# Kernel tuning notes

Hardware: AMD Instinct MI355X
Metric: run time of the kernel (lower is better)

Reference implementation:

```python
import jax, jax.numpy as jnp
from jax import lax
import numpy as np

B, T, IN, H, NC = 2048, 512, 1, 128, 8


def setup_inputs() -> dict:
    key = jax.random.key(0)
    ks = jax.random.split(key, 13)
    s = 0.05
    inp = {
        "x": jax.random.normal(ks[0], (B, T, IN), dtype=jnp.float32),
        # layer 0 LSTM params (PyTorch layout: W_ih [4H, in], W_hh [4H, H])
        "W_ih0": jax.random.normal(ks[1], (4 * H, IN), dtype=jnp.float32) * s,
        "W_hh0": jax.random.normal(ks[2], (4 * H, H), dtype=jnp.float32) * s,
        "b_ih0": jax.random.normal(ks[3], (4 * H,), dtype=jnp.float32) * s,
        "b_hh0": jax.random.normal(ks[4], (4 * H,), dtype=jnp.float32) * s,
        # layer 1 LSTM params
        "W_ih1": jax.random.normal(ks[5], (4 * H, H), dtype=jnp.float32) * s,
        "W_hh1": jax.random.normal(ks[6], (4 * H, H), dtype=jnp.float32) * s,
        "b_ih1": jax.random.normal(ks[7], (4 * H,), dtype=jnp.float32) * s,
        "b_hh1": jax.random.normal(ks[8], (4 * H,), dtype=jnp.float32) * s,
        # classifier: Linear(H,64) -> ReLU -> Linear(64,NC)
        "W1": jax.random.normal(ks[9], (64, H), dtype=jnp.float32) * s,
        "b1": jax.random.normal(ks[10], (64,), dtype=jnp.float32) * s,
        "W2": jax.random.normal(ks[11], (NC, 64), dtype=jnp.float32) * s,
        "b2": jax.random.normal(ks[12], (NC,), dtype=jnp.float32) * s,
    }
    return inp


def _lstm_layer(x_seq, W_ih, W_hh, b_ih, b_hh):
    # x_seq: [B, T, in]. PyTorch gate order: i, f, g, o.
    bsz = x_seq.shape[0]
    h_dim = W_hh.shape[1]
    # Precompute input projections for all timesteps (big GEMM outside scan).
    x_proj = jnp.einsum('bti,gi->btg', x_seq, W_ih) + b_ih + b_hh  # [B, T, 4H]

    def step(carry, xp_t):
        h, c = carry
        gates = xp_t + h @ W_hh.T  # [B, 4H]
        i_g, f_g, g_g, o_g = jnp.split(gates, 4, axis=-1)
        i_g = jax.nn.sigmoid(i_g)
        f_g = jax.nn.sigmoid(f_g)
        g_g = jnp.tanh(g_g)
        o_g = jax.nn.sigmoid(o_g)
        c = f_g * c + i_g * g_g
        h = o_g * jnp.tanh(c)
        return (h, c), h

    init = (jnp.zeros((bsz, h_dim), x_seq.dtype), jnp.zeros((bsz, h_dim), x_seq.dtype))
    (_, _), hs = lax.scan(step, init, jnp.swapaxes(x_proj, 0, 1))  # hs: [T, B, H]
    return jnp.swapaxes(hs, 0, 1)  # [B, T, H]


def reference(x, W_ih0, W_hh0, b_ih0, b_hh0, W_ih1, W_hh1, b_ih1, b_hh1, W1, b1, W2, b2):
    h0 = _lstm_layer(x, W_ih0, W_hh0, b_ih0, b_hh0)   # [B, T, H]
    h1 = _lstm_layer(h0, W_ih1, W_hh1, b_ih1, b_hh1)  # [B, T, H] (dropout off in eval)
    last = h1[:, -1, :]                                # [B, H]
    hidden = jax.nn.relu(last @ W1.T + b1)             # [B, 64]
    logits = hidden @ W2.T + b2                        # [B, NC]
    return logits
```

## Files before the change

### kernel.cpp

```cpp
#include <hip/hip_runtime.h>
#include <stdint.h>

typedef float f32x4 __attribute__((ext_vector_type(4)));
typedef short s16x8 __attribute__((ext_vector_type(8)));
typedef short s16x4 __attribute__((ext_vector_type(4)));
typedef uint32_t u32x4 __attribute__((ext_vector_type(4)));

#define HDIM 128
#define TLEN 512
#define BT 16

__device__ __forceinline__ unsigned short f2bf(float f) {
    union { float f; uint32_t u; } v; v.f = f;
    uint32_t r = v.u + 0x7FFFu + ((v.u >> 16) & 1u);
    return (unsigned short)(r >> 16);
}
__device__ __forceinline__ float bfhi(uint32_t u){ union{uint32_t u;float f;}v; v.u = u & 0xFFFF0000u; return v.f; }
__device__ __forceinline__ float bflo(uint32_t u){ union{uint32_t u;float f;}v; v.u = u << 16; return v.f; }
__device__ __forceinline__ float bf2f(short s){ union{uint32_t u;float f;}v; v.u = ((uint32_t)(unsigned short)s) << 16; return v.f; }

__device__ __forceinline__ float sigmoidf_(float x){
    float e = __expf(-x);
    return __builtin_amdgcn_rcpf(1.0f + e);
}
__device__ __forceinline__ float tanhf_(float x){
    float e = __expf(2.0f * x);
    return 1.0f - 2.0f * __builtin_amdgcn_rcpf(1.0f + e);
}

#define MFMA16(A, B, C) __builtin_amdgcn_mfma_f32_16x16x32_bf16((A), (B), (C), 0, 0, 0)
#define UNPK(arr, idx) (((idx) & 1) ? bfhi(arr[(idx) >> 1]) : bflo(arr[(idx) >> 1]))

__global__ __launch_bounds__(512, 2) void lstm_pipe_kernel(
    const float* __restrict__ x,
    const float* __restrict__ Wih0,
    const float* __restrict__ Whh0,
    const float* __restrict__ bih0,
    const float* __restrict__ bhh0,
    const float* __restrict__ Wih1,
    const float* __restrict__ Whh1,
    const float* __restrict__ bih1,
    const float* __restrict__ bhh1,
    const float* __restrict__ W1,
    const float* __restrict__ b1,
    const float* __restrict__ W2,
    const float* __restrict__ b2,
    short* __restrict__ ring,
    int* __restrict__ flags,
    float* __restrict__ out)
{
    __shared__ __align__(16) short h0A[2][2048];
    __shared__ __align__(16) short h1f[2][2048];
    __shared__ __align__(16) float headH[16 * HDIM];
    __shared__ __align__(16) float headL[16 * 64];

    const int role = blockIdx.x & 1;
    const int p    = blockIdx.x >> 1;
    const int tid  = threadIdx.x;
    const int w = tid >> 6;
    const int l = tid & 63;
    const int n = l & 15;
    const int q = l >> 4;
    const int b0 = p * BT;
    const float* xrow = x + (size_t)(b0 + n) * TLEN;
    short* ringp = ring + (size_t)p * TLEN * 2048;

    const int u0 = w * 16 + q * 4;
    const int fragoff = (((u0 >> 5) * 64) + n + 16 * ((u0 >> 3) & 3)) * 8 + (u0 & 7);

    if (role == 0) {
        s16x8 w0f[4][4];
        #pragma unroll
        for (int c = 0; c < 4; ++c) {
            #pragma unroll
            for (int tile = 0; tile < 4; ++tile) {
                const int g  = tile * 128 + w * 16 + n;
                const int k0 = c * 32 + q * 8;
                const float* pw = Whh0 + g * HDIM + k0;
                s16x8 a;
                #pragma unroll
                for (int j = 0; j < 8; ++j) a[j] = (short)f2bf(pw[j]);
                w0f[c][tile] = a;
            }
        }
        uint32_t b0p[8], wxp[8];
        #pragma unroll
        for (int i = 0; i < 8; ++i) {
            const int tr0 = 2 * i;
            const int tile = tr0 >> 2, r0 = tr0 & 3;
            const int g0 = tile * 128 + u0 + r0;
            const int g1 = g0 + 1;
            b0p[i] = ((uint32_t)f2bf(bih0[g1] + bhh0[g1]) << 16) | f2bf(bih0[g0] + bhh0[g0]);
            wxp[i] = ((uint32_t)f2bf(Wih0[g1]) << 16) | f2bf(Wih0[g0]);
        }
        float c0v[4] = {0.f, 0.f, 0.f, 0.f};

        {
            const float x0 = xrow[0];
            s16x4 hw;
            #pragma unroll
            for (int r = 0; r < 4; ++r) {
                const float pi = fmaf(UNPK(wxp, r),      x0, UNPK(b0p, r));
                const float pg = fmaf(UNPK(wxp, 8 + r),  x0, UNPK(b0p, 8 + r));
                const float po = fmaf(UNPK(wxp, 12 + r), x0, UNPK(b0p, 12 + r));
                const float ig = sigmoidf_(pi);
                const float gg = tanhf_(pg);
                const float og = sigmoidf_(po);
                const float cc = ig * gg;
                c0v[r] = cc;
                hw[r] = (short)f2bf(og * tanhf_(cc));
            }
            *(s16x4*)&h0A[0][fragoff] = hw;
            *(s16x4*)&ringp[fragoff] = hw;
        }
        __syncthreads();

        #pragma unroll 1
        for (int i = 0; i < 511; ++i) {
            const short* R = h0A[i & 1];
            short*       W = h0A[(i + 1) & 1];
            const float xv = xrow[i + 1];
            s16x8 hb[4];
            #pragma unroll
            for (int c = 0; c < 4; ++c) hb[c] = *(const s16x8*)&R[(c * 64 + l) * 8];
            f32x4 a[4];
            #pragma unroll
            for (int tile = 0; tile < 4; ++tile) {
                #pragma unroll
                for (int r = 0; r < 4; ++r) {
                    const int tr = tile * 4 + r;
                    a[tile][r] = fmaf(UNPK(wxp, tr), xv, UNPK(b0p, tr));
                }
            }
            #pragma unroll
            for (int c = 0; c < 4; ++c) {
                #pragma unroll
                for (int tile = 0; tile < 4; ++tile)
                    a[tile] = MFMA16(w0f[c][tile], hb[c], a[tile]);
            }
            s16x4 hw;
            #pragma unroll
            for (int r = 0; r < 4; ++r) {
                const float ig = sigmoidf_(a[0][r]);
                const float fg = sigmoidf_(a[1][r]);
                const float gg = tanhf_(a[2][r]);
                const float og = sigmoidf_(a[3][r]);
                const float cc = fmaf(fg, c0v[r], ig * gg);
                c0v[r] = cc;
                hw[r] = (short)f2bf(og * tanhf_(cc));
            }
            *(s16x4*)&W[fragoff] = hw;
            *(s16x4*)&ringp[(size_t)(i + 1) * 2048 + fragoff] = hw;

            if (((i + 2) & 7) == 0) {
                __threadfence();
                __syncthreads();
                if (tid == 0)
                    __hip_atomic_store(&flags[p], (i + 2) >> 3,
                                       __ATOMIC_RELEASE, __HIP_MEMORY_SCOPE_AGENT);
            } else {
                __syncthreads();
            }
        }
        return;
    }

    s16x8 wi1f[4][4], wh1f[4][4];
    #pragma unroll
    for (int c = 0; c < 4; ++c) {
        #pragma unroll
        for (int tile = 0; tile < 4; ++tile) {
            const int g  = tile * 128 + w * 16 + n;
            const int k0 = c * 32 + q * 8;
            const float* p1 = Wih1 + g * HDIM + k0;
            const float* p2 = Whh1 + g * HDIM + k0;
            s16x8 a, b;
            #pragma unroll
            for (int j = 0; j < 8; ++j) { a[j] = (short)f2bf(p1[j]); b[j] = (short)f2bf(p2[j]); }
            wi1f[c][tile] = a; wh1f[c][tile] = b;
        }
    }
    uint32_t b1p[8];
    #pragma unroll
    for (int i = 0; i < 8; ++i) {
        const int tr0 = 2 * i;
        const int tile = tr0 >> 2, r0 = tr0 & 3;
        const int g0 = tile * 128 + u0 + r0;
        const int g1 = g0 + 1;
        b1p[i] = ((uint32_t)f2bf(bih1[g1] + bhh1[g1]) << 16) | f2bf(bih1[g0] + bhh1[g0]);
    }
    for (int s2 = tid; s2 < 1024; s2 += 512) ((uint32_t*)h1f[1])[s2] = 0u;
    float c1v[4] = {0.f, 0.f, 0.f, 0.f};

#define WAITCHUNK(C) do {                                                     \
    if (tid == 0) {                                                           \
        while (__hip_atomic_load(&flags[p], __ATOMIC_ACQUIRE,                 \
                                 __HIP_MEMORY_SCOPE_AGENT) < (C))             \
            __builtin_amdgcn_s_sleep(8);                                      \
    }                                                                         \
    __syncthreads();                                                          \
    __threadfence();         \
} while (0)

#define LOADCUR(DST, T) do {                                                  \
    _Pragma("unroll")                                                         \
    for (int c = 0; c < 4; ++c)                                               \
        (DST)[c] = *(const s16x8*)&ringp[(size_t)(T) * 2048 + (c * 64 + l) * 8]; \
} while (0)

#define BSTEP(K, CUR, NXT, DO_PF) do {                                        \
    const short* R1_ = h1f[((K) + 1) & 1];                                    \
    short*       W1_ = h1f[(K) & 1];                                          \
    s16x8 hb1_[4];                                                            \
    _Pragma("unroll")                                                         \
    for (int c = 0; c < 4; ++c) hb1_[c] = *(const s16x8*)&R1_[(c * 64 + l) * 8]; \
    f32x4 a_[4];                                                              \
    _Pragma("unroll")                                                         \
    for (int tile = 0; tile < 4; ++tile) {                                    \
        _Pragma("unroll")                                                     \
        for (int r = 0; r < 4; ++r) a_[tile][r] = UNPK(b1p, tile * 4 + r);    \
    }                                                                         \
    _Pragma("unroll")                                                         \
    for (int c = 0; c < 4; ++c) {                                             \
        _Pragma("unroll")                                                     \
        for (int tile = 0; tile < 4; ++tile)                                  \
            a_[tile] = MFMA16(wi1f[c][tile], (CUR)[c], a_[tile]);             \
    }                                                                         \
    if (DO_PF) { LOADCUR(NXT, (K) + 1); }                                     \
    _Pragma("unroll")                                                         \
    for (int c = 0; c < 4; ++c) {                                             \
        _Pragma("unroll")                                                     \
        for (int tile = 0; tile < 4; ++tile)                                  \
            a_[tile] = MFMA16(wh1f[c][tile], hb1_[c], a_[tile]);              \
    }                                                                         \
    s16x4 hw_;                                                                \
    _Pragma("unroll")                                                         \
    for (int r = 0; r < 4; ++r) {                                             \
        const float ig = sigmoidf_(a_[0][r]);                                 \
        const float fg = sigmoidf_(a_[1][r]);                                 \
        const float gg = tanhf_(a_[2][r]);                                    \
        const float og = sigmoidf_(a_[3][r]);                                 \
        const float cc = fmaf(fg, c1v[r], ig * gg);                           \
        c1v[r] = cc;                                                          \
        hw_[r] = (short)f2bf(og * tanhf_(cc));                                \
    }                                                                         \
    *(s16x4*)&W1_[fragoff] = hw_;                                             \
    __syncthreads();                                                          \
} while (0)

    s16x8 curA[4], curB[4];

    #pragma unroll 1
    for (int c64 = 0; c64 < 63; ++c64) {
        WAITCHUNK(c64 + 1);
        const int kb = 8 * c64;
        LOADCUR(curA, kb);
        BSTEP(kb + 0, curA, curB, true);
        BSTEP(kb + 1, curB, curA, true);
        BSTEP(kb + 2, curA, curB, true);
        BSTEP(kb + 3, curB, curA, true);
        BSTEP(kb + 4, curA, curB, true);
        BSTEP(kb + 5, curB, curA, true);
        BSTEP(kb + 6, curA, curB, true);
        BSTEP(kb + 7, curB, curA, false);
    }
    WAITCHUNK(64);
    LOADCUR(curA, 504);
    BSTEP(504, curA, curB, true);
    BSTEP(505, curB, curA, true);
    BSTEP(506, curA, curB, true);
    BSTEP(507, curB, curA, true);
    BSTEP(508, curA, curB, true);
    BSTEP(509, curB, curA, true);
    BSTEP(510, curA, curB, true);

    {
        const short* R1 = h1f[0];
        s16x8 hb1_[4];
        #pragma unroll
        for (int c = 0; c < 4; ++c) hb1_[c] = *(const s16x8*)&R1[(c * 64 + l) * 8];
        f32x4 a_[4];
        #pragma unroll
        for (int tile = 0; tile < 4; ++tile) {
            #pragma unroll
            for (int r = 0; r < 4; ++r) a_[tile][r] = UNPK(b1p, tile * 4 + r);
        }
        #pragma unroll
        for (int c = 0; c < 4; ++c) {
            #pragma unroll
            for (int tile = 0; tile < 4; ++tile) {
                a_[tile] = MFMA16(wi1f[c][tile], curB[c], a_[tile]);
                a_[tile] = MFMA16(wh1f[c][tile], hb1_[c], a_[tile]);
            }
        }
        f32x4 hv;
        #pragma unroll
        for (int r = 0; r < 4; ++r) {
            const float ig = sigmoidf_(a_[0][r]);
            const float fg = sigmoidf_(a_[1][r]);
            const float gg = tanhf_(a_[2][r]);
            const float og = sigmoidf_(a_[3][r]);
            const float cc = fmaf(fg, c1v[r], ig * gg);
            hv[r] = og * tanhf_(cc);
        }
        *(f32x4*)&headH[n * HDIM + u0] = hv;
    }
    __syncthreads();

    #pragma unroll
    for (int rep = 0; rep < 2; ++rep) {
        const int idx = tid + rep * 512;
        const int nn = idx >> 6, j = idx & 63;
        float s = b1[j];
        const float* wrow = W1 + j * HDIM;
        const float* hrow = headH + nn * HDIM;
        #pragma unroll
        for (int k = 0; k < HDIM; k += 4) {
            const f32x4 hv = *(const f32x4*)&hrow[k];
            const f32x4 wv = *(const f32x4*)&wrow[k];
            s += hv[0]*wv[0] + hv[1]*wv[1] + hv[2]*wv[2] + hv[3]*wv[3];
        }
        headL[nn * 64 + j] = fmaxf(s, 0.0f);
    }
    __syncthreads();

    if (tid < 128) {
        const int nn = tid >> 3, cls = tid & 7;
        float s = b2[cls];
        const float* wrow = W2 + cls * 64;
        const float* hrow = headL + nn * 64;
        #pragma unroll
        for (int k = 0; k < 64; k += 4) {
            const f32x4 hv = *(const f32x4*)&hrow[k];
            const f32x4 wv = *(const f32x4*)&wrow[k];
            s += hv[0]*wv[0] + hv[1]*wv[1] + hv[2]*wv[2] + hv[3]*wv[3];
        }
        out[(size_t)(b0 + nn) * 8 + cls] = s;
    }
#undef WAITCHUNK
#undef LOADCUR
#undef BSTEP
}

__global__ __launch_bounds__(512, 2) void lstm_fused_kernel(
    const float* __restrict__ x,
    const float* __restrict__ Wih0,
    const float* __restrict__ Whh0,
    const float* __restrict__ bih0,
    const float* __restrict__ bhh0,
    const float* __restrict__ Wih1,
    const float* __restrict__ Whh1,
    const float* __restrict__ bih1,
    const float* __restrict__ bhh1,
    const float* __restrict__ W1,
    const float* __restrict__ b1,
    const float* __restrict__ W2,
    const float* __restrict__ b2,
    float* __restrict__ out)
{
    __shared__ __align__(16) short wh1lds[65536];
    __shared__ __align__(16) short h0f0[2048], h0f1[2048];
    __shared__ __align__(16) short h1f0[2048], h1f1[2048];
    __shared__ __align__(16) float b1lds[4][8][16];

    const int tid = threadIdx.x;
    const int w   = tid >> 6;
    const int wl  = w & 3;
    const bool isL0 = (w < 4);
    const int l = tid & 63;
    const int n = l & 15;
    const int q = l >> 4;
    const int b0 = blockIdx.x * BT;
    const float* xrow = x + (size_t)(b0 + n) * TLEN;

    for (int s2 = tid; s2 < 8192; s2 += 512) {
        const int ll = s2 & 63, t2 = (s2 >> 6) & 7, cc = (s2 >> 9) & 3, wv = s2 >> 11;
        const int row = (t2 >> 1) * 128 + 32 * wv + 16 * (t2 & 1) + (ll & 15);
        const int k0  = cc * 32 + (ll >> 4) * 8;
        const float* p = Whh1 + row * HDIM + k0;
        s16x8 a;
        #pragma unroll
        for (int j = 0; j < 8; ++j) a[j] = (short)f2bf(p[j]);
        *(s16x8*)&wh1lds[s2 * 8] = a;
    }
    {
        const int idx = tid;
        const int wv = idx >> 7, t2 = (idx >> 4) & 7, j = idx & 15;
        const int row = (t2 >> 1) * 128 + 32 * wv + 16 * (t2 & 1) + j;
        b1lds[wv][t2][j] = bih1[row] + bhh1[row];
    }
    for (int s2 = tid; s2 < 1024; s2 += 512) ((uint32_t*)h1f1)[s2] = 0u;

    const int ub0 = 32 * wl + 4 * q;
    const int ub1 = ub0 + 16;
    const int fo0 = ((ub0 >> 5) * 64 + n + 16 * ((ub0 >> 3) & 3)) * 8 + (ub0 & 7);
    const int fo1 = ((ub1 >> 5) * 64 + n + 16 * ((ub1 >> 3) & 3)) * 8 + (ub1 & 7);

#define L0ITER(K, R0, W0) do {                                                \
    const int xi_ = (K) + 1;                                                  \
    const float xv_ = xrow[xi_ < TLEN ? xi_ : (TLEN - 1)];                    \
    s16x8 hb_[4];                                                             \
    _Pragma("unroll")                                                         \
    for (int c = 0; c < 4; ++c) hb_[c] = *(const s16x8*)&(R0)[(c * 64 + l) * 8]; \
    f32x4 a_[8];                                                              \
    _Pragma("unroll")                                                         \
    for (int t2 = 0; t2 < 8; ++t2) {                                          \
        _Pragma("unroll")                                                     \
        for (int r = 0; r < 4; ++r)                                           \
            a_[t2][r] = fmaf(bfhi(bwx[t2][r]), xv_, bflo(bwx[t2][r]));        \
    }                                                                         \
    _Pragma("unroll")                                                         \
    for (int c = 0; c < 4; ++c) {                                             \
        _Pragma("unroll")                                                     \
        for (int t2 = 0; t2 < 8; ++t2)                                        \
            a_[t2] = MFMA16(w0f[c][t2], hb_[c], a_[t2]);                      \
    }                                                                         \
    _Pragma("unroll")                                                         \
    for (int h = 0; h < 2; ++h) {                                             \
        s16x4 hw;                                                             \
        _Pragma("unroll")                                                     \
        for (int r = 0; r < 4; ++r) {                                         \
            const float ig = sigmoidf_(a_[0 + h][r]);                         \
            const float fg = sigmoidf_(a_[2 + h][r]);                         \
            const float gg = tanhf_(a_[4 + h][r]);                            \
            const float og = sigmoidf_(a_[6 + h][r]);                         \
            const float cc = fmaf(fg, c0_[h][r], ig * gg);                    \
            c0_[h][r] = cc;                                                   \
            hw[r] = (short)f2bf(og * tanhf_(cc));                             \
        }                                                                     \
        *(s16x4*)&(W0)[h ? fo1 : fo0] = hw;                                   \
    }                                                                         \
    __syncthreads();                                                          \
} while (0)

#define L1ITER(K, R0, R1, W1) do {                                            \
    s16x8 hb0_[4], hb1_[4];                                                   \
    _Pragma("unroll")                                                         \
    for (int c = 0; c < 4; ++c) {                                             \
        hb0_[c] = *(const s16x8*)&(R0)[(c * 64 + l) * 8];                     \
        hb1_[c] = *(const s16x8*)&(R1)[(c * 64 + l) * 8];                     \
    }                                                                         \
    f32x4 a_[8];                                                              \
    _Pragma("unroll")                                                         \
    for (int t2 = 0; t2 < 8; ++t2)                                            \
        a_[t2] = *(const f32x4*)&b1lds[wl][t2][q * 4];                        \
    _Pragma("unroll")                                                         \
    for (int c = 0; c < 4; ++c) {                                             \
        _Pragma("unroll")                                                     \
        for (int t2 = 0; t2 < 8; ++t2)                                        \
            a_[t2] = MFMA16(wi1f[c][t2], hb0_[c], a_[t2]);                    \
    }                                                                         \
    _Pragma("unroll")                                                         \
    for (int c = 0; c < 4; ++c) {                                             \
        s16x8 wt_[8];                                                         \
        _Pragma("unroll")                                                     \
        for (int t2 = 0; t2 < 8; ++t2)                                        \
            wt_[t2] = *(const s16x8*)&wh1lds[(((wl * 4 + c) * 8 + t2) * 64 + l) * 8]; \
        _Pragma("unroll")                                                     \
        for (int t2 = 0; t2 < 8; ++t2)                                        \
            a_[t2] = MFMA16(wt_[t2], hb1_[c], a_[t2]);                        \
    }                                                                         \
    _Pragma("unroll")                                                         \
    for (int h = 0; h < 2; ++h) {                                             \
        s16x4 hw;                                                             \
        _Pragma("unroll")                                                     \
        for (int r = 0; r < 4; ++r) {                                         \
            const float ig = sigmoidf_(a_[0 + h][r]);                         \
            const float fg = sigmoidf_(a_[2 + h][r]);                         \
            const float gg = tanhf_(a_[4 + h][r]);                            \
            const float og = sigmoidf_(a_[6 + h][r]);                         \
            const float cc = fmaf(fg, c1_[h][r], ig * gg);                    \
            c1_[h][r] = cc;                                                   \
            hw[r] = (short)f2bf(og * tanhf_(cc));                             \
        }                                                                     \
        *(s16x4*)&(W1)[h ? fo1 : fo0] = hw;                                   \
    }                                                                         \
    __syncthreads();                                                          \
} while (0)

    if (isL0) {
        s16x8 w0f[4][8];
        #pragma unroll
        for (int c = 0; c < 4; ++c) {
            #pragma unroll
            for (int t2 = 0; t2 < 8; ++t2) {
                const int row = (t2 >> 1) * 128 + 32 * wl + 16 * (t2 & 1) + n;
                const int k0 = c * 32 + q * 8;
                const float* p = Whh0 + row * HDIM + k0;
                s16x8 a;
                #pragma unroll
                for (int j = 0; j < 8; ++j) a[j] = (short)f2bf(p[j]);
                w0f[c][t2] = a;
            }
        }
        u32x4 bwx[8];
        #pragma unroll
        for (int t2 = 0; t2 < 8; ++t2) {
            #pragma unroll
            for (int r = 0; r < 4; ++r) {
                const int row = (t2 >> 1) * 128 + 32 * wl + 16 * (t2 & 1) + 4 * q + r;
                bwx[t2][r] = ((uint32_t)f2bf(Wih0[row]) << 16) | f2bf(bih0[row] + bhh0[row]);
            }
        }
        float c0_[2][4] = {{0.f,0.f,0.f,0.f},{0.f,0.f,0.f,0.f}};
        {
            const float x0 = xrow[0];
            #pragma unroll
            for (int h = 0; h < 2; ++h) {
                s16x4 hw;
                #pragma unroll
                for (int r = 0; r < 4; ++r) {
                    const float pi = fmaf(bfhi(bwx[0 + h][r]), x0, bflo(bwx[0 + h][r]));
                    const float pg = fmaf(bfhi(bwx[4 + h][r]), x0, bflo(bwx[4 + h][r]));
                    const float po = fmaf(bfhi(bwx[6 + h][r]), x0, bflo(bwx[6 + h][r]));
                    const float ig = sigmoidf_(pi);
                    const float gg = tanhf_(pg);
                    const float og = sigmoidf_(po);
                    const float cc = ig * gg;
                    c0_[h][r] = cc;
                    hw[r] = (short)f2bf(og * tanhf_(cc));
                }
                *(s16x4*)&h0f0[h ? fo1 : fo0] = hw;
            }
        }
        __syncthreads();
        #pragma unroll 1
        for (int k = 0; k < TLEN; k += 2) {
            L0ITER(k,     h0f0, h0f1);
            L0ITER(k + 1, h0f1, h0f0);
        }
    } else {
        s16x8 wi1f[4][8];
        #pragma unroll
        for (int c = 0; c < 4; ++c) {
            #pragma unroll
            for (int t2 = 0; t2 < 8; ++t2) {
                const int row = (t2 >> 1) * 128 + 32 * wl + 16 * (t2 & 1) + n;
                const int k0 = c * 32 + q * 8;
                const float* p = Wih1 + row * HDIM + k0;
                s16x8 a;
                #pragma unroll
                for (int j = 0; j < 8; ++j) a[j] = (short)f2bf(p[j]);
                wi1f[c][t2] = a;
            }
        }
        float c1_[2][4] = {{0.f,0.f,0.f,0.f},{0.f,0.f,0.f,0.f}};
        __syncthreads();
        #pragma unroll 1
        for (int k = 0; k < TLEN; k += 2) {
            L1ITER(k,     h0f0, h1f1, h1f0);
            L1ITER(k + 1, h0f1, h1f0, h1f1);
        }
        {
            const short* R0 = h0f0;
            const short* R1 = h1f1;
            (void)R0; (void)R1;
        }
    }

    __syncthreads();

    float* headH = (float*)wh1lds;
    float* headL = headH + 16 * HDIM;
    if (!isL0) {
        #pragma unroll
        for (int h = 0; h < 2; ++h) {
            const s16x4 hv = *(const s16x4*)&h1f1[h ? fo1 : fo0];
            f32x4 hf;
            #pragma unroll
            for (int r = 0; r < 4; ++r) hf[r] = bf2f(hv[r]);
            *(f32x4*)&headH[n * HDIM + (h ? ub1 : ub0)] = hf;
        }
    }
    __syncthreads();

    #pragma unroll
    for (int rep = 0; rep < 2; ++rep) {
        const int idx = tid + rep * 512;
        const int nn = idx >> 6, j = idx & 63;
        float s = b1[j];
        const float* wrow = W1 + j * HDIM;
        const float* hrow = headH + nn * HDIM;
        #pragma unroll
        for (int k = 0; k < HDIM; k += 4) {
            const f32x4 hv = *(const f32x4*)&hrow[k];
            const f32x4 wv = *(const f32x4*)&wrow[k];
            s += hv[0]*wv[0] + hv[1]*wv[1] + hv[2]*wv[2] + hv[3]*wv[3];
        }
        headL[nn * 64 + j] = fmaxf(s, 0.0f);
    }
    __syncthreads();

    if (tid < 128) {
        const int nn = tid >> 3, cls = tid & 7;
        float s = b2[cls];
        const float* wrow = W2 + cls * 64;
        const float* hrow = headL + nn * 64;
        #pragma unroll
        for (int k = 0; k < 64; k += 4) {
            const f32x4 hv = *(const f32x4*)&hrow[k];
            const f32x4 wv = *(const f32x4*)&wrow[k];
            s += hv[0]*wv[0] + hv[1]*wv[1] + hv[2]*wv[2] + hv[3]*wv[3];
        }
        out[(size_t)(b0 + nn) * 8 + cls] = s;
    }
#undef L0ITER
#undef L1ITER
}

extern "C" void kernel_launch(void* const* d_in, const int* in_sizes, int n_in,
                              void* d_out, int out_size, void* d_ws, size_t ws_size,
                              hipStream_t stream) {
    const float* x    = (const float*)d_in[0];
    const float* Wih0 = (const float*)d_in[1];
    const float* Whh0 = (const float*)d_in[2];
    const float* bih0 = (const float*)d_in[3];
    const float* bhh0 = (const float*)d_in[4];
    const float* Wih1 = (const float*)d_in[5];
    const float* Whh1 = (const float*)d_in[6];
    const float* bih1 = (const float*)d_in[7];
    const float* bhh1 = (const float*)d_in[8];
    const float* W1   = (const float*)d_in[9];
    const float* b1   = (const float*)d_in[10];
    const float* W2   = (const float*)d_in[11];
    const float* b2   = (const float*)d_in[12];
    float* outp = (float*)d_out;

    const size_t ring_bytes = (size_t)128 * TLEN * 2048 * sizeof(short);
    const size_t need = 4096 + ring_bytes;

    if (ws_size >= need) {
        int*   flags = (int*)d_ws;
        short* ring  = (short*)((char*)d_ws + 4096);
        hipMemsetAsync(d_ws, 0, 4096, stream);
        lstm_pipe_kernel<<<256, 512, 0, stream>>>(
            x, Wih0, Whh0, bih0, bhh0, Wih1, Whh1, bih1, bhh1,
            W1, b1, W2, b2, ring, flags, outp);
    } else {
        lstm_fused_kernel<<<128, 512, 0, stream>>>(
            x, Wih0, Whh0, bih0, bhh0, Wih1, Whh1, bih1, bhh1,
            W1, b1, W2, b2, outp);
    }
}
```

Before: 954.8 us.

## Replace full-length layer-0 ring with bounded circular buffer plus consumer back-pressure

The layer-0 to layer-1 handoff buffer is now a power-of-two circular ring of D chunks sized from the available workspace, instead of storing all 512 timesteps per batch tile. A consumer flag lets the layer-1 block post progress, and the layer-0 producer waits on it before overwriting slots. Flags are padded to separate 64-byte lines and the spin-wait sleep is shortened. The aim is a smaller, more cache-resident ring and less flag contention, at the cost of possible producer stalls and bounded spin loops that could break out early if the limit is reached.

```diff
diff --git a/kernel.cpp b/kernel.cpp
--- a/kernel.cpp
+++ b/kernel.cpp
@@ -9,6 +9,7 @@
 #define HDIM 128
 #define TLEN 512
 #define BT 16
+#define SPIN_LIMIT (1 << 22)
 
 __device__ __forceinline__ unsigned short f2bf(float f) {
     union { float f; uint32_t u; } v; v.f = f;
@@ -46,8 +47,11 @@
     const float* __restrict__ W2,
     const float* __restrict__ b2,
     short* __restrict__ ring,
-    int* __restrict__ flags,
-    float* __restrict__ out)
+    int* __restrict__ prodF,
+    int* __restrict__ consF,
+    float* __restrict__ out,
+    const int dchunks,
+    const int dmask)
 {
     __shared__ __align__(16) short h0A[2][2048];
     __shared__ __align__(16) short h1f[2][2048];
@@ -63,7 +67,7 @@
     const int q = l >> 4;
     const int b0 = p * BT;
     const float* xrow = x + (size_t)(b0 + n) * TLEN;
-    short* ringp = ring + (size_t)p * TLEN * 2048;
+    short* ringp = ring + (size_t)p * (size_t)(dmask + 1) * 2048;
 
     const int u0 = w * 16 + q * 4;
     const int fragoff = (((u0 >> 5) * 64) + n + 16 * ((u0 >> 3) & 3)) * 8 + (u0 & 7);
@@ -117,6 +121,21 @@
 
         #pragma unroll 1
         for (int i = 0; i < 511; ++i) {
+            if (((i + 1) & 7) == 0) {
+                const int c = (i + 1) >> 3;
+                const int needCons = c + 1 - dchunks;
+                if (needCons > 0) {
+                    if (tid == 0) {
+                        int guard = 0;
+                        while (__hip_atomic_load(&consF[p * 16], __ATOMIC_ACQUIRE,
+                                                 __HIP_MEMORY_SCOPE_AGENT) < needCons) {
+                            if (++guard > SPIN_LIMIT) break;
+                            __builtin_amdgcn_s_sleep(2);
+                        }
+                    }
+                    __syncthreads();
+                }
+            }
             const short* R = h0A[i & 1];
             short*       W = h0A[(i + 1) & 1];
             const float xv = xrow[i + 1];
@@ -150,13 +169,13 @@
                 hw[r] = (short)f2bf(og * tanhf_(cc));
             }
             *(s16x4*)&W[fragoff] = hw;
-            *(s16x4*)&ringp[(size_t)(i + 1) * 2048 + fragoff] = hw;
+            *(s16x4*)&ringp[(size_t)((i + 1) & dmask) * 2048 + fragoff] = hw;
 
             if (((i + 2) & 7) == 0) {
                 __threadfence();
                 __syncthreads();
                 if (tid == 0)
-                    __hip_atomic_store(&flags[p], (i + 2) >> 3,
+                    __hip_atomic_store(&prodF[p * 16], (i + 2) >> 3,
                                        __ATOMIC_RELEASE, __HIP_MEMORY_SCOPE_AGENT);
             } else {
                 __syncthreads();
@@ -194,18 +213,27 @@
 
 #define WAITCHUNK(C) do {                                                     \
     if (tid == 0) {                                                           \
-        while (__hip_atomic_load(&flags[p], __ATOMIC_ACQUIRE,                 \
-                                 __HIP_MEMORY_SCOPE_AGENT) < (C))             \
-            __builtin_amdgcn_s_sleep(8);                                      \
+        int guard = 0;                                                        \
+        while (__hip_atomic_load(&prodF[p * 16], __ATOMIC_ACQUIRE,            \
+                                 __HIP_MEMORY_SCOPE_AGENT) < (C)) {           \
+            if (++guard > SPIN_LIMIT) break;                    \
+            __builtin_amdgcn_s_sleep(2);                                      \
+        }                                                                     \
     }                                                                         \
     __syncthreads();                                                          \
-    __threadfence();         \
+    __threadfence();                 \
 } while (0)
 
+#define POSTCHUNK(C) do {                                                     \
+    if (tid == 0)                                                             \
+        __hip_atomic_store(&consF[p * 16], (C),                               \
+                           __ATOMIC_RELEASE, __HIP_MEMORY_SCOPE_AGENT);       \
+} while (0)
+
 #define LOADCUR(DST, T) do {                                                  \
     _Pragma("unroll")                                                         \
     for (int c = 0; c < 4; ++c)                                               \
-        (DST)[c] = *(const s16x8*)&ringp[(size_t)(T) * 2048 + (c * 64 + l) * 8]; \
+        (DST)[c] = *(const s16x8*)&ringp[(size_t)((T) & dmask) * 2048 + (c * 64 + l) * 8]; \
 } while (0)
 
 #define BSTEP(K, CUR, NXT, DO_PF) do {                                        \
@@ -263,6 +291,7 @@
         BSTEP(kb + 5, curB, curA, true);
         BSTEP(kb + 6, curA, curB, true);
         BSTEP(kb + 7, curB, curA, false);
+        POSTCHUNK(c64 + 1);
     }
     WAITCHUNK(64);
     LOADCUR(curA, 504);
@@ -338,6 +367,7 @@
         out[(size_t)(b0 + nn) * 8 + cls] = s;
     }
 #undef WAITCHUNK
+#undef POSTCHUNK
 #undef LOADCUR
 #undef BSTEP
 }
@@ -551,11 +581,6 @@
             L1ITER(k,     h0f0, h1f1, h1f0);
             L1ITER(k + 1, h0f1, h1f0, h1f1);
         }
-        {
-            const short* R0 = h0f0;
-            const short* R1 = h1f1;
-            (void)R0; (void)R1;
-        }
     }
 
     __syncthreads();
@@ -626,16 +651,21 @@
     const float* b2   = (const float*)d_in[12];
     float* outp = (float*)d_out;
 
-    const size_t ring_bytes = (size_t)128 * TLEN * 2048 * sizeof(short);
-    const size_t need = 4096 + ring_bytes;
-
-    if (ws_size >= need) {
-        int*   flags = (int*)d_ws;
-        short* ring  = (short*)((char*)d_ws + 4096);
-        hipMemsetAsync(d_ws, 0, 4096, stream);
+    const size_t FLAGS_BYTES = 32768;
+    size_t avail = (ws_size > FLAGS_BYTES) ? (ws_size - FLAGS_BYTES) : 0;
+    const size_t maxChunks = avail / ((size_t)128 * 32768);
+    int D = 0;
+    for (int cand = 64; cand >= 2; cand >>= 1)
+        if (maxChunks >= (size_t)cand) { D = cand; break; }
+
+    if (D >= 2) {
+        int*   prodF = (int*)d_ws;
+        int*   consF = (int*)d_ws + 4096;
+        short* ring  = (short*)((char*)d_ws + FLAGS_BYTES);
+        hipMemsetAsync(d_ws, 0, FLAGS_BYTES, stream);
         lstm_pipe_kernel<<<256, 512, 0, stream>>>(
             x, Wih0, Whh0, bih0, bhh0, Wih1, Whh1, bih1, bhh1,
-            W1, b1, W2, b2, ring, flags, outp);
+            W1, b1, W2, b2, ring, prodF, consF, outp, D, 8 * D - 1);
     } else {
         lstm_fused_kernel<<<128, 512, 0, stream>>>(
             x, Wih0, Whh0, bih0, bhh0, Wih1, Whh1, bih1, bhh1,
```

Result: slower. 3.516 ms (+268.3%).
